# Kernel tuning notes

Measured on AMD Instinct MI355X. Metric: run time of the kernel, lower is better.

Reference implementation:

```python
import jax, jax.numpy as jnp
import numpy as np

DIST_THRESHOLD = 900.0  # distance_threshold from __init__
NO_CODE_ID = -1         # no_code_id from __init__


def setup_inputs() -> dict:
    key = jax.random.key(0)
    k1, k2 = jax.random.split(key)
    x = jax.random.normal(k1, (4, 2048, 512), dtype=jnp.float32)      # [b, n, d] tokens
    codes = jax.random.normal(k2, (16384, 512), dtype=jnp.float32)    # [c, d] full codebook
    return {"x": x, "codes": codes}


def reference(x, codes):
    x2 = jnp.sum(x * x, axis=-1, keepdims=True)            # [b, n, 1]
    c2 = jnp.sum(codes * codes, axis=-1)                   # [c]
    xc = jnp.einsum('bnd,cd->bnc', x, codes)               # [b, n, c] (the compute-heavy GEMM)
    dist_sq = jnp.maximum(x2 + c2 - 2.0 * xc, 0.0)         # clamp tiny negatives, like cdist

    within = jnp.any(dist_sq <= DIST_THRESHOLD, axis=-1)   # [b, n]
    nn_ids = jnp.argmin(dist_sq, axis=-1)                  # [b, n]
    ids = jnp.where(within, nn_ids, NO_CODE_ID)            # tokens outside threshold -> no_code_id
    return ids
```

## Files before the change

### kernel.cpp

```cpp
#include <hip/hip_runtime.h>


#define NTOK   8192
#define NCODES 16384
#define DDIM   512
#define NCHUNK 16
#define CHUNK  1024
#define DIST_THR 900.0f

typedef unsigned short u16;
typedef _Float16 half8 __attribute__((ext_vector_type(8)));
typedef float    f32x4 __attribute__((ext_vector_type(4)));

__device__ __forceinline__ void conv_body(const float* __restrict__ src,
                                          u16* __restrict__ dh,
                                          u16* __restrict__ dl, int c) {
    int r = c & 15, q = (c >> 4) & 3, g = (c >> 6) & 7, kit = (c >> 9) & 15;
    int tile = c >> 13;
    int row = tile * 128 + g * 16 + r;
    int k = kit * 32 + q * 8;
    const float* p = src + (size_t)row * DDIM + k;
    float4 v0 = *(const float4*)p;
    float4 v1 = *(const float4*)(p + 4);
    float vv[8] = {v0.x, v0.y, v0.z, v0.w, v1.x, v1.y, v1.z, v1.w};
    u16 hs[8], ls[8];
    #pragma unroll
    for (int j = 0; j < 8; ++j) {
        float sv = vv[j] * 16.0f;
        _Float16 h = (_Float16)sv;
        float hf = (float)h;
        _Float16 l = (_Float16)(sv - hf);
        union { _Float16 f; u16 u; } uh, ul;
        uh.f = h; ul.f = l;
        hs[j] = uh.u; ls[j] = ul.u;
    }
    uint4 H, L;
    H.x = hs[0] | ((unsigned)hs[1] << 16); H.y = hs[2] | ((unsigned)hs[3] << 16);
    H.z = hs[4] | ((unsigned)hs[5] << 16); H.w = hs[6] | ((unsigned)hs[7] << 16);
    L.x = ls[0] | ((unsigned)ls[1] << 16); L.y = ls[2] | ((unsigned)ls[3] << 16);
    L.z = ls[4] | ((unsigned)ls[5] << 16); L.w = ls[6] | ((unsigned)ls[7] << 16);
    *(uint4*)(dh + (size_t)c * 8) = H;
    *(uint4*)(dl + (size_t)c * 8) = L;
}

__global__ __launch_bounds__(256) void nn_prep(const float* __restrict__ x,
                                               const float* __restrict__ codes,
                                               u16* __restrict__ xh, u16* __restrict__ xl,
                                               u16* __restrict__ ch, u16* __restrict__ cl,
                                               float* __restrict__ c2) {
    int b = blockIdx.x;
    if (b < 2048) {
        conv_body(x, xh, xl, b * 256 + threadIdx.x);
    } else if (b < 6144) {
        conv_body(codes, ch, cl, (b - 2048) * 256 + threadIdx.x);
    } else {
        int w = threadIdx.x >> 6;
        int lane = threadIdx.x & 63;
        int c = (b - 6144) * 4 + w;
        const float* p = codes + (size_t)c * DDIM + lane * 8;
        float4 v0 = *(const float4*)p;
        float4 v1 = *(const float4*)(p + 4);
        float s = v0.x*v0.x + v0.y*v0.y + v0.z*v0.z + v0.w*v0.w
                + v1.x*v1.x + v1.y*v1.y + v1.z*v1.z + v1.w*v1.w;
        #pragma unroll
        for (int off = 32; off > 0; off >>= 1) s += __shfl_down(s, off);
        if (lane == 0) c2[c] = s;
    }
}

__global__ __launch_bounds__(256, 2) void nn_gemm(const u16* __restrict__ xh,
                                                  const u16* __restrict__ xl,
                                                  const u16* __restrict__ chh,
                                                  const u16* __restrict__ cll,
                                                  const float* __restrict__ c2,
                                                  float* __restrict__ pmin,
                                                  int* __restrict__ pid) {
    __shared__ __align__(16) char smem[49152];
    const int tid = threadIdx.x;
    const int lane = tid & 63;
    const int wave = tid >> 6;
    const int wm = wave & 1;
    const int wn = wave >> 1;
    const int mtile = blockIdx.x >> 4;
    const int chunk = blockIdx.x & 15;
    const int m0 = mtile * 128;

    float mv[16];
    int   mi[16];
    #pragma unroll
    for (int s = 0; s < 16; ++s) { mv[s] = 3.4e38f; mi[s] = 0; }

    for (int nt = 0; nt < 4; ++nt) {
        f32x4 acc[4][8];
        #pragma unroll
        for (int i = 0; i < 4; ++i)
            #pragma unroll
            for (int j = 0; j < 8; ++j) acc[i][j] = (f32x4)0.0f;

        for (int kit = 0; kit < 16; ++kit) {
            #pragma unroll
            for (int s = 0; s < 12; ++s) {
                int g = wave * 12 + s;
                const u16* gsrc;
                if (g < 16) {
                    const u16* base = (g < 8) ? xh : xl;
                    gsrc = base + ((size_t)(mtile * 16 + kit)) * 4096
                                + (size_t)(g & 7) * 512;
                } else {
                    int h = g - 16;
                    const u16* base = (h < 16) ? chh : cll;
                    int ct = (h >> 3) & 1;
                    gsrc = base + ((size_t)((chunk * 8 + nt * 2 + ct) * 16 + kit)) * 4096
                                + (size_t)(h & 7) * 512;
                }
                __builtin_amdgcn_global_load_lds(
                    (const __attribute__((address_space(1))) void*)(gsrc + lane * 8),
                    (__attribute__((address_space(3))) void*)(smem + g * 1024),
                    16, 0, 0);
            }
            __syncthreads();

            const char* Ah = smem;
            const char* Al = smem + 8192;
            const char* Bh = smem + 16384;
            const char* Bl = smem + 32768;
            half8 ah[4], al[4];
            #pragma unroll
            for (int i = 0; i < 4; ++i) {
                int g = wm * 4 + i;
                ah[i] = *(const half8*)(Ah + g * 1024 + lane * 16);
                al[i] = *(const half8*)(Al + g * 1024 + lane * 16);
            }
            #pragma unroll
            for (int j = 0; j < 8; ++j) {
                int g = wn * 8 + j;
                half8 bh = *(const half8*)(Bh + g * 1024 + lane * 16);
                half8 bl = *(const half8*)(Bl + g * 1024 + lane * 16);
                #pragma unroll
                for (int i = 0; i < 4; ++i) {
                    acc[i][j] = __builtin_amdgcn_mfma_f32_16x16x32_f16(ah[i], bh, acc[i][j], 0, 0, 0);
                    acc[i][j] = __builtin_amdgcn_mfma_f32_16x16x32_f16(ah[i], bl, acc[i][j], 0, 0, 0);
                    acc[i][j] = __builtin_amdgcn_mfma_f32_16x16x32_f16(al[i], bh, acc[i][j], 0, 0, 0);
                }
            }
            __syncthreads();
        }

        #pragma unroll
        for (int j = 0; j < 8; ++j) {
            int ncol = nt * 256 + wn * 128 + j * 16 + (lane & 15);
            int gid = chunk * CHUNK + ncol;
            float cv = c2[gid];
            #pragma unroll
            for (int i = 0; i < 4; ++i)
                #pragma unroll
                for (int r = 0; r < 4; ++r) {
                    float s = fmaf(acc[i][j][r], -0.0078125f, cv);
                    int slot = i * 4 + r;
                    if (s < mv[slot]) { mv[slot] = s; mi[slot] = gid; }
                }
        }
    }

    #pragma unroll
    for (int off = 1; off < 16; off <<= 1) {
        #pragma unroll
        for (int s = 0; s < 16; ++s) {
            float ov = __shfl_xor(mv[s], off);
            int   oi = __shfl_xor(mi[s], off);
            if (ov < mv[s] || (ov == mv[s] && oi < mi[s])) { mv[s] = ov; mi[s] = oi; }
        }
    }
    if ((lane & 15) == 0) {
        #pragma unroll
        for (int i = 0; i < 4; ++i)
            #pragma unroll
            for (int r = 0; r < 4; ++r) {
                int row = wm * 64 + i * 16 + (lane >> 4) * 4 + r;
                int2 e;
                e.x = __float_as_int(mv[i * 4 + r]);
                e.y = mi[i * 4 + r];
                *(int2*)(smem + (wn * 128 + row) * 8) = e;
            }
    }
    __syncthreads();
    if (tid < 128) {
        int2 e0 = *(const int2*)(smem + tid * 8);
        int2 e1 = *(const int2*)(smem + (128 + tid) * 8);
        float v0 = __int_as_float(e0.x), v1 = __int_as_float(e1.x);
        float bv = v0; int bi = e0.y;
        if (v1 < bv || (v1 == bv && e1.y < bi)) { bv = v1; bi = e1.y; }
        pmin[(size_t)(m0 + tid) * NCHUNK + chunk] = bv;
        pid [(size_t)(m0 + tid) * NCHUNK + chunk] = bi;
    }
}

__global__ __launch_bounds__(256) void nn_fin(const float* __restrict__ x,
                                              const float* __restrict__ pmin,
                                              const int* __restrict__ pid,
                                              int* __restrict__ out) {
    int w = threadIdx.x >> 6;
    int lane = threadIdx.x & 63;
    int t = blockIdx.x * 4 + w;
    const float* p = x + (size_t)t * DDIM + lane * 8;
    float4 v0 = *(const float4*)p;
    float4 v1 = *(const float4*)(p + 4);
    float s = v0.x*v0.x + v0.y*v0.y + v0.z*v0.z + v0.w*v0.w
            + v1.x*v1.x + v1.y*v1.y + v1.z*v1.z + v1.w*v1.w;
    #pragma unroll
    for (int off = 32; off > 0; off >>= 1) s += __shfl_down(s, off);
    if (lane == 0) {
        const float* pm = pmin + (size_t)t * NCHUNK;
        const int*   pi = pid  + (size_t)t * NCHUNK;
        float bv = pm[0]; int bi = pi[0];
        #pragma unroll
        for (int c = 1; c < NCHUNK; ++c) {
            float v = pm[c]; int id = pi[c];
            if (v < bv || (v == bv && id < bi)) { bv = v; bi = id; }
        }
        float mind = s + bv;
        out[t] = (mind <= DIST_THR) ? bi : -1;
    }
}

extern "C" void kernel_launch(void* const* d_in, const int* in_sizes, int n_in,
                              void* d_out, int out_size, void* d_ws, size_t ws_size,
                              hipStream_t stream) {
    const float* x     = (const float*)d_in[0];
    const float* codes = (const float*)d_in[1];
    int* out = (int*)d_out;

    char* ws = (char*)d_ws;
    u16*   xh   = (u16*)(ws);
    u16*   xl   = (u16*)(ws + 8388608);
    u16*   chh  = (u16*)(ws + 16777216);
    u16*   cll  = (u16*)(ws + 33554432);
    float* c2   = (float*)(ws + 50331648);
    float* pmin = (float*)(ws + 50397184);
    int*   pid  = (int*)  (ws + 50921472);

    nn_prep<<<10240, 256, 0, stream>>>(x, codes, xh, xl, chh, cll, c2);
    nn_gemm<<<64 * NCHUNK, 256, 0, stream>>>(xh, xl, chh, cll, c2, pmin, pid);
    nn_fin<<<NTOK / 4, 256, 0, stream>>>(x, pmin, pid, out);
}
```

Measured before the change: 430.6 us.

## Enlarge GEMM tiles to 256x256 with double-buffered LDS prefetch pipeline

```diff
diff --git a/kernel.cpp b/kernel.cpp
--- a/kernel.cpp
+++ b/kernel.cpp
@@ -4,8 +4,8 @@
 #define NTOK   8192
 #define NCODES 16384
 #define DDIM   512
-#define NCHUNK 16
-#define CHUNK  1024
+#define NCHUNK 8
+#define CHUNK  2048
 #define DIST_THR 900.0f
 
 typedef unsigned short u16;
@@ -68,98 +68,110 @@
     }
 }
 
-__global__ __launch_bounds__(256, 2) void nn_gemm(const u16* __restrict__ xh,
+__global__ __launch_bounds__(512, 2) void nn_gemm(const u16* __restrict__ xh,
                                                   const u16* __restrict__ xl,
                                                   const u16* __restrict__ chh,
                                                   const u16* __restrict__ cll,
                                                   const float* __restrict__ c2,
                                                   float* __restrict__ pmin,
                                                   int* __restrict__ pid) {
-    __shared__ __align__(16) char smem[49152];
+    __shared__ __align__(16) char smem[131072];
     const int tid = threadIdx.x;
     const int lane = tid & 63;
     const int wave = tid >> 6;
-    const int wm = wave & 1;
-    const int wn = wave >> 1;
-    const int mtile = blockIdx.x >> 4;
-    const int chunk = blockIdx.x & 15;
-    const int m0 = mtile * 128;
+    const int wm = wave & 3;
+    const int wn = wave >> 2;
+    const int mtile = blockIdx.x >> 3;
+    const int chunk = blockIdx.x & 7;
+    const int m0 = mtile * 256;
+
+    const int plane = wave >> 1;
+    const int tsub  = wave & 1;
+    const bool isA = (plane < 2);
+    const u16* gbase;
+    if (plane == 0)      gbase = xh  + ((size_t)(mtile * 2 + tsub) * 16) * 4096;
+    else if (plane == 1) gbase = xl  + ((size_t)(mtile * 2 + tsub) * 16) * 4096;
+    else if (plane == 2) gbase = chh + ((size_t)(chunk * 16 + tsub) * 16) * 4096;
+    else                 gbase = cll + ((size_t)(chunk * 16 + tsub) * 16) * 4096;
+    gbase += lane * 8;
+    const int ldsoff = wave * 8192;
 
     float mv[16];
     int   mi[16];
     #pragma unroll
     for (int s = 0; s < 16; ++s) { mv[s] = 3.4e38f; mi[s] = 0; }
 
-    for (int nt = 0; nt < 4; ++nt) {
-        f32x4 acc[4][8];
-        #pragma unroll
-        for (int i = 0; i < 4; ++i)
-            #pragma unroll
-            for (int j = 0; j < 8; ++j) acc[i][j] = (f32x4)0.0f;
-
-        for (int kit = 0; kit < 16; ++kit) {
-            #pragma unroll
-            for (int s = 0; s < 12; ++s) {
-                int g = wave * 12 + s;
-                const u16* gsrc;
-                if (g < 16) {
-                    const u16* base = (g < 8) ? xh : xl;
-                    gsrc = base + ((size_t)(mtile * 16 + kit)) * 4096
-                                + (size_t)(g & 7) * 512;
-                } else {
-                    int h = g - 16;
-                    const u16* base = (h < 16) ? chh : cll;
-                    int ct = (h >> 3) & 1;
-                    gsrc = base + ((size_t)((chunk * 8 + nt * 2 + ct) * 16 + kit)) * 4096
-                                + (size_t)(h & 7) * 512;
-                }
-                __builtin_amdgcn_global_load_lds(
-                    (const __attribute__((address_space(1))) void*)(gsrc + lane * 8),
-                    (__attribute__((address_space(3))) void*)(smem + g * 1024),
-                    16, 0, 0);
+    f32x4 acc[4][8];
+    #pragma unroll
+    for (int i = 0; i < 4; ++i)
+        #pragma unroll
+        for (int j = 0; j < 8; ++j) acc[i][j] = (f32x4)0.0f;
+
+    auto stage = [&](int it2) {
+        int kit2 = it2 & 15, nt2 = it2 >> 4;
+        size_t off = (size_t)(isA ? kit2 : nt2 * 32 + kit2) * 4096;
+        const u16* src = gbase + off;
+        char* dst = smem + (size_t)(it2 & 1) * 65536 + ldsoff;
+        #pragma unroll
+        for (int s = 0; s < 8; ++s)
+            __builtin_amdgcn_global_load_lds(
+                (const __attribute__((address_space(1))) void*)(src + s * 512),
+                (__attribute__((address_space(3))) void*)(dst + s * 1024),
+                16, 0, 0);
+    };
+
+    stage(0);
+    for (int it = 0; it < 128; ++it) {
+        if (it < 127) {
+            stage(it + 1);
+            asm volatile("s_waitcnt vmcnt(8)\n\ts_barrier" ::: "memory");
+        } else {
+            asm volatile("s_waitcnt vmcnt(0)\n\ts_barrier" ::: "memory");
+        }
+
+        const char* cur = smem + (size_t)(it & 1) * 65536;
+        half8 ah[4], al[4];
+        #pragma unroll
+        for (int i = 0; i < 4; ++i) {
+            int g = wm * 4 + i;
+            ah[i] = *(const half8*)(cur +         g * 1024 + lane * 16);
+            al[i] = *(const half8*)(cur + 16384 + g * 1024 + lane * 16);
+        }
+        #pragma unroll
+        for (int j = 0; j < 8; ++j) {
+            int g = wn * 8 + j;
+            half8 bh = *(const half8*)(cur + 32768 + g * 1024 + lane * 16);
+            half8 bl = *(const half8*)(cur + 49152 + g * 1024 + lane * 16);
+            #pragma unroll
+            for (int i = 0; i < 4; ++i) {
+                acc[i][j] = __builtin_amdgcn_mfma_f32_16x16x32_f16(ah[i], bh, acc[i][j], 0, 0, 0);
+                acc[i][j] = __builtin_amdgcn_mfma_f32_16x16x32_f16(ah[i], bl, acc[i][j], 0, 0, 0);
+                acc[i][j] = __builtin_amdgcn_mfma_f32_16x16x32_f16(al[i], bh, acc[i][j], 0, 0, 0);
             }
-            __syncthreads();
-
-            const char* Ah = smem;
-            const char* Al = smem + 8192;
-            const char* Bh = smem + 16384;
-            const char* Bl = smem + 32768;
-            half8 ah[4], al[4];
-            #pragma unroll
-            for (int i = 0; i < 4; ++i) {
-                int g = wm * 4 + i;
-                ah[i] = *(const half8*)(Ah + g * 1024 + lane * 16);
-                al[i] = *(const half8*)(Al + g * 1024 + lane * 16);
+        }
+
+        if ((it & 15) == 15) {
+            int nt = it >> 4;
+            #pragma unroll
+            for (int j = 0; j < 8; ++j) {
+                int ncol = nt * 256 + wn * 128 + j * 16 + (lane & 15);
+                int gid = chunk * CHUNK + ncol;
+                float cv = c2[gid];
+                #pragma unroll
+                for (int i = 0; i < 4; ++i)
+                    #pragma unroll
+                    for (int r = 0; r < 4; ++r) {
+                        float s = fmaf(acc[i][j][r], -0.0078125f, cv);
+                        int slot = i * 4 + r;
+                        if (s < mv[slot]) { mv[slot] = s; mi[slot] = gid; }
+                    }
             }
-            #pragma unroll
-            for (int j = 0; j < 8; ++j) {
-                int g = wn * 8 + j;
-                half8 bh = *(const half8*)(Bh + g * 1024 + lane * 16);
-                half8 bl = *(const half8*)(Bl + g * 1024 + lane * 16);
-                #pragma unroll
-                for (int i = 0; i < 4; ++i) {
-                    acc[i][j] = __builtin_amdgcn_mfma_f32_16x16x32_f16(ah[i], bh, acc[i][j], 0, 0, 0);
-                    acc[i][j] = __builtin_amdgcn_mfma_f32_16x16x32_f16(ah[i], bl, acc[i][j], 0, 0, 0);
-                    acc[i][j] = __builtin_amdgcn_mfma_f32_16x16x32_f16(al[i], bh, acc[i][j], 0, 0, 0);
-                }
-            }
-            __syncthreads();
-        }
-
-        #pragma unroll
-        for (int j = 0; j < 8; ++j) {
-            int ncol = nt * 256 + wn * 128 + j * 16 + (lane & 15);
-            int gid = chunk * CHUNK + ncol;
-            float cv = c2[gid];
             #pragma unroll
             for (int i = 0; i < 4; ++i)
                 #pragma unroll
-                for (int r = 0; r < 4; ++r) {
-                    float s = fmaf(acc[i][j][r], -0.0078125f, cv);
-                    int slot = i * 4 + r;
-                    if (s < mv[slot]) { mv[slot] = s; mi[slot] = gid; }
-                }
-        }
+                for (int j = 0; j < 8; ++j) acc[i][j] = (f32x4)0.0f;
+        }
+        asm volatile("s_barrier" ::: "memory");
     }
 
     #pragma unroll
@@ -180,13 +192,13 @@
                 int2 e;
                 e.x = __float_as_int(mv[i * 4 + r]);
                 e.y = mi[i * 4 + r];
-                *(int2*)(smem + (wn * 128 + row) * 8) = e;
+                *(int2*)(smem + (wn * 256 + row) * 8) = e;
             }
     }
     __syncthreads();
-    if (tid < 128) {
+    if (tid < 256) {
         int2 e0 = *(const int2*)(smem + tid * 8);
-        int2 e1 = *(const int2*)(smem + (128 + tid) * 8);
+        int2 e1 = *(const int2*)(smem + (256 + tid) * 8);
         float v0 = __int_as_float(e0.x), v1 = __int_as_float(e1.x);
         float bv = v0; int bi = e0.y;
         if (v1 < bv || (v1 == bv && e1.y < bi)) { bv = v1; bi = e1.y; }
@@ -237,9 +249,9 @@
     u16*   cll  = (u16*)(ws + 33554432);
     float* c2   = (float*)(ws + 50331648);
     float* pmin = (float*)(ws + 50397184);
-    int*   pid  = (int*)  (ws + 50921472);
+    int*   pid  = (int*)  (ws + 50659328);
 
     nn_prep<<<10240, 256, 0, stream>>>(x, codes, xh, xl, chh, cll, c2);
-    nn_gemm<<<64 * NCHUNK, 256, 0, stream>>>(xh, xl, chh, cll, c2, pmin, pid);
+    nn_gemm<<<32 * NCHUNK, 512, 0, stream>>>(xh, xl, chh, cll, c2, pmin, pid);
     nn_fin<<<NTOK / 4, 256, 0, stream>>>(x, pmin, pid, out);
 }
```

Measured after the change: 408.3 us. -5.2%, faster.
